# Kernel optimization log

Measured on AMD Instinct MI355X. Metric: run time of the kernel, lower is better.

Reference implementation:

```python
import jax, jax.numpy as jnp
import numpy as np

L = 12        # depth
DIM = 768     # model dim
HEADS = 12
DHEAD = 64
INNER = HEADS * DHEAD   # 768
MLP = 3072
P = 16        # patch size
IMG = 384
C = 3
B = 16
NCLS = 1000
NPATCH = (IMG // P) ** 2   # 576
N = NPATCH + 1             # 577 (cls token)
PATCH_DIM = C * P * P      # 768
SCALE = DIM ** (-0.5)      # NOTE: original scales by dim, not dim_head


def setup_inputs() -> dict:
    key = jax.random.key(0)
    ks = jax.random.split(key, 21)
    rn = lambda k, shape, s=0.02: jax.random.normal(k, shape, dtype=jnp.float32) * s
    return {
        "img": jax.random.normal(ks[0], (B, C, IMG, IMG), dtype=jnp.float32),
        "patch_w": rn(ks[1], (PATCH_DIM, DIM)),
        "patch_b": rn(ks[2], (DIM,)),
        "pos_emb": rn(ks[3], (1, N, DIM), 1.0),
        "cls_tok": rn(ks[4], (1, 1, DIM), 1.0),
        "ln1_w": jnp.ones((L, DIM), jnp.float32),
        "ln1_b": jnp.zeros((L, DIM), jnp.float32),
        "qkv_w": rn(ks[5], (L, DIM, 3 * INNER)),
        "out_w": rn(ks[6], (L, INNER, DIM)),
        "out_b": rn(ks[7], (L, DIM)),
        "ln2_w": jnp.ones((L, DIM), jnp.float32),
        "ln2_b": jnp.zeros((L, DIM), jnp.float32),
        "ff1_w": rn(ks[8], (L, DIM, MLP)),
        "ff1_b": rn(ks[9], (L, MLP)),
        "ff2_w": rn(ks[10], (L, MLP, DIM)),
        "ff2_b": rn(ks[11], (L, DIM)),
        "head_ln_w": jnp.ones((DIM,), jnp.float32),
        "head_ln_b": jnp.zeros((DIM,), jnp.float32),
        "head_w": rn(ks[12], (DIM, NCLS)),
        "head_b": rn(ks[13], (NCLS,)),
    }


def layer_norm(x, w, b, eps=1e-5):
    mu = jnp.mean(x, axis=-1, keepdims=True)
    var = jnp.mean(jnp.square(x - mu), axis=-1, keepdims=True)
    return (x - mu) * jax.lax.rsqrt(var + eps) * w + b


def _vit_forward(img, patch_w, patch_b, pos_emb, cls_tok,
                 ln1_w, ln1_b, qkv_w, out_w, out_b,
                 ln2_w, ln2_b, ff1_w, ff1_b, ff2_w, ff2_b,
                 head_ln_w, head_ln_b, head_w, head_b):
    b = img.shape[0]
    g = IMG // P
    # rearrange 'b c (h p1) (w p2) -> b (h w) (p1 p2 c)'
    x = img.reshape(b, C, g, P, g, P).transpose(0, 2, 4, 3, 5, 1).reshape(b, NPATCH, PATCH_DIM)
    x = x @ patch_w + patch_b                           # [b, 576, dim]
    cls = jnp.broadcast_to(cls_tok, (b, 1, DIM))
    x = jnp.concatenate([cls, x], axis=1) + pos_emb[:, :N]   # [b, 577, dim]

    def block(x, p):
        l1w, l1b, qkvw, ow, ob, l2w, l2b, f1w, f1b, f2w, f2b = p
        # attention (pre-norm, residual inside Attention.forward)
        h = layer_norm(x, l1w, l1b)
        qkv = h @ qkvw                                  # [b, n, 3*inner]
        q, k, v = jnp.split(qkv, 3, axis=-1)
        to_heads = lambda t: t.reshape(b, N, HEADS, DHEAD).transpose(0, 2, 1, 3)
        q, k, v = to_heads(q), to_heads(k), to_heads(v)  # [b, h, n, d]
        dots = jnp.einsum('bhid,bhjd->bhij', q, k) * SCALE
        attn = jax.nn.softmax(dots, axis=-1)
        o = jnp.einsum('bhij,bhjd->bhid', attn, v)
        o = o.transpose(0, 2, 1, 3).reshape(b, N, INNER)
        x = x + (o @ ow + ob)
        # feedforward (pre-norm, residual)
        h2 = layer_norm(x, l2w, l2b)
        h2 = jax.nn.gelu(h2 @ f1w + f1b, approximate=False)
        x = x + (h2 @ f2w + f2b)
        return x, None

    x, _ = jax.lax.scan(block, x,
                        (ln1_w, ln1_b, qkv_w, out_w, out_b,
                         ln2_w, ln2_b, ff1_w, ff1_b, ff2_w, ff2_b))
    cls_out = x[:, 0]                                   # [b, dim]
    return layer_norm(cls_out, head_ln_w, head_ln_b) @ head_w + head_b


def reference(img, patch_w, patch_b, pos_emb, cls_tok,
              ln1_w, ln1_b, qkv_w, out_w, out_b,
              ln2_w, ln2_b, ff1_w, ff1_b, ff2_w, ff2_b,
              head_ln_w, head_ln_b, head_w, head_b):
    return _vit_forward(img, patch_w, patch_b, pos_emb, cls_tok,
                        ln1_w, ln1_b, qkv_w, out_w, out_b,
                        ln2_w, ln2_b, ff1_w, ff1_b, ff2_w, ff2_b,
                        head_ln_w, head_ln_b, head_w, head_b)
```

## Files before the change

### kernel.cpp

```cpp
#include <hip/hip_runtime.h>
#include <cstdint>


typedef __attribute__((ext_vector_type(8))) short bf16x8;
typedef __attribute__((ext_vector_type(4))) float f32x4;

#define NTOK 577

__device__ __forceinline__ ushort f2bf(float f) {
  union { float f; unsigned int u; } x; x.f = f;
  unsigned int r = x.u + 0x7fffu + ((x.u >> 16) & 1u);
  return (ushort)(r >> 16);
}

__device__ __forceinline__ void gload_lds16(const ushort* g, ushort* l) {
  __builtin_amdgcn_global_load_lds(
      (const __attribute__((address_space(1))) unsigned int*)g,
      (__attribute__((address_space(3))) unsigned int*)l, 16, 0, 0);
}

__global__ __launch_bounds__(256) void convt_kernel(const float* __restrict__ W,
                                                    ushort* __restrict__ Wt,
                                                    int K, int N) {
  __shared__ float t[32][33];
  const int kb = blockIdx.x * 32, nb = blockIdx.y * 32;
  const int tx = threadIdx.x & 31, ty = threadIdx.x >> 5;
#pragma unroll
  for (int i = 0; i < 32; i += 8)
    t[ty + i][tx] = W[(size_t)(kb + ty + i) * N + (nb + tx)];
  __syncthreads();
#pragma unroll
  for (int i = 0; i < 32; i += 8)
    Wt[(size_t)(nb + ty + i) * K + (kb + tx)] = f2bf(t[tx][ty + i]);
}

__global__ __launch_bounds__(256) void im2col_kernel(const float* __restrict__ img,
                                                     ushort* __restrict__ Ap) {
  const int idx = blockIdx.x * 256 + threadIdx.x;
  const int j = idx % 768;
  const int m = idx / 768;
  const int c = j % 3;
  const int q = j / 3;
  const int px = q & 15, py = q >> 4;
  const int b = m / 576, p = m % 576;
  const int gy = p / 24, gx = p % 24;
  const float v = img[((size_t)(b * 3 + c) * 384 + (gy * 16 + py)) * 384 + (gx * 16 + px)];
  Ap[idx] = f2bf(v);
}

__global__ void clspos_kernel(const float* __restrict__ cls_tok,
                              const float* __restrict__ pos,
                              float* __restrict__ x) {
  const int i = blockIdx.x * 256 + threadIdx.x;
  const int b = i / 768, d = i % 768;
  x[(size_t)b * NTOK * 768 + d] = cls_tok[d] + pos[d];
}

__global__ __launch_bounds__(64) void ln_kernel(const float* __restrict__ x,
                                                const float* __restrict__ w,
                                                const float* __restrict__ bb,
                                                ushort* __restrict__ out) {
  const int row = blockIdx.x, lane = threadIdx.x;
  const float4* xr = reinterpret_cast<const float4*>(x + (size_t)row * 768);
  const float4 v0 = xr[lane], v1 = xr[lane + 64], v2 = xr[lane + 128];
  float vals[12] = {v0.x, v0.y, v0.z, v0.w, v1.x, v1.y, v1.z, v1.w,
                    v2.x, v2.y, v2.z, v2.w};
  float s = 0.f;
#pragma unroll
  for (int i = 0; i < 12; ++i) s += vals[i];
#pragma unroll
  for (int o = 32; o; o >>= 1) s += __shfl_xor(s, o);
  const float mu = s * (1.0f / 768.0f);
  float q = 0.f;
#pragma unroll
  for (int i = 0; i < 12; ++i) { const float d = vals[i] - mu; q += d * d; }
#pragma unroll
  for (int o = 32; o; o >>= 1) q += __shfl_xor(q, o);
  const float rstd = rsqrtf(q * (1.0f / 768.0f) + 1e-5f);
  const float4* w4 = reinterpret_cast<const float4*>(w);
  const float4* b4 = reinterpret_cast<const float4*>(bb);
  ushort* orow = out + (size_t)row * 768;
#pragma unroll
  for (int ch = 0; ch < 3; ++ch) {
    const float4 wv = w4[lane + ch * 64];
    const float4 bv = b4[lane + ch * 64];
    ushort4 u;
    u.x = f2bf((vals[ch * 4 + 0] - mu) * rstd * wv.x + bv.x);
    u.y = f2bf((vals[ch * 4 + 1] - mu) * rstd * wv.y + bv.y);
    u.z = f2bf((vals[ch * 4 + 2] - mu) * rstd * wv.z + bv.z);
    u.w = f2bf((vals[ch * 4 + 3] - mu) * rstd * wv.w + bv.w);
    *reinterpret_cast<ushort4*>(orow + ch * 256 + lane * 4) = u;
  }
}

constexpr int EPI_BF16 = 0;
constexpr int EPI_GELU_BF16 = 1;
constexpr int EPI_RES_F32 = 2;
constexpr int EPI_PATCH = 3;

template <int EPI>
__global__ __launch_bounds__(256) void gemm_kernel(
    const ushort* __restrict__ A, const ushort* __restrict__ Bt,
    const float* __restrict__ bias, const float* __restrict__ extra,
    void* __restrict__ Cptr, int M, int N, int K) {
  __shared__ ushort Alds[128 * 32];
  __shared__ ushort Blds[128 * 32];
  const int tid = threadIdx.x;
  const int tileM = blockIdx.x * 128, tileN = blockIdx.y * 128;
  const int wave = tid >> 6, lane = tid & 63;
  const int wrow = (wave >> 1) * 64, wcol = (wave & 1) * 64;
  const int lr = lane & 15, lk = (lane >> 4) * 8;

  f32x4 acc[4][4];
#pragma unroll
  for (int m = 0; m < 4; ++m)
#pragma unroll
    for (int n = 0; n < 4; ++n) acc[m][n] = (f32x4){0.f, 0.f, 0.f, 0.f};

  const int srow = wave * 32 + (lane >> 2);
  const int scol = (lane & 3) * 8;
  const ushort* Ap = A + (size_t)(tileM + srow) * K + scol;
  const ushort* Bp = Bt + (size_t)(tileN + srow) * K + scol;
  ushort* Al0 = &Alds[(wave * 2 + 0) * 512];
  ushort* Al1 = &Alds[(wave * 2 + 1) * 512];
  ushort* Bl0 = &Blds[(wave * 2 + 0) * 512];
  ushort* Bl1 = &Blds[(wave * 2 + 1) * 512];
  const size_t cstride = (size_t)16 * K;

  for (int k0 = 0; k0 < K; k0 += 32) {
    __syncthreads();
    gload_lds16(Ap + k0, Al0);
    gload_lds16(Ap + k0 + cstride, Al1);
    gload_lds16(Bp + k0, Bl0);
    gload_lds16(Bp + k0 + cstride, Bl1);
    __syncthreads();

    bf16x8 af[4], bfr[4];
#pragma unroll
    for (int m = 0; m < 4; ++m)
      af[m] = *reinterpret_cast<const bf16x8*>(&Alds[(wrow + m * 16 + lr) * 32 + lk]);
#pragma unroll
    for (int n = 0; n < 4; ++n)
      bfr[n] = *reinterpret_cast<const bf16x8*>(&Blds[(wcol + n * 16 + lr) * 32 + lk]);
#pragma unroll
    for (int m = 0; m < 4; ++m)
#pragma unroll
      for (int n = 0; n < 4; ++n)
        acc[m][n] = __builtin_amdgcn_mfma_f32_16x16x32_bf16(af[m], bfr[n],
                                                            acc[m][n], 0, 0, 0);
  }

  const int lr4 = (lane >> 4) * 4;
#pragma unroll
  for (int m = 0; m < 4; ++m) {
#pragma unroll
    for (int r = 0; r < 4; ++r) {
      const int row = tileM + wrow + m * 16 + lr4 + r;
      if (row >= M) continue;
#pragma unroll
      for (int n = 0; n < 4; ++n) {
        const int col = tileN + wcol + n * 16 + lr;
        float v = acc[m][n][r];
        if constexpr (EPI == EPI_BF16) {
          reinterpret_cast<ushort*>(Cptr)[(size_t)row * N + col] = f2bf(v);
        } else if constexpr (EPI == EPI_GELU_BF16) {
          v += bias[col];
          v = 0.5f * v * (1.0f + erff(v * 0.70710678118654752440f));
          reinterpret_cast<ushort*>(Cptr)[(size_t)row * N + col] = f2bf(v);
        } else if constexpr (EPI == EPI_RES_F32) {
          v += bias[col] + extra[(size_t)row * N + col];
          reinterpret_cast<float*>(Cptr)[(size_t)row * N + col] = v;
        } else {
          const int bb = row / 576;
          const int p = row - bb * 576;
          v += bias[col] + extra[(size_t)(p + 1) * 768 + col];
          reinterpret_cast<float*>(Cptr)[(size_t)(row + bb + 1) * 768 + col] = v;
        }
      }
    }
  }
}

__global__ __launch_bounds__(256) void attn_kernel(const ushort* __restrict__ qkv,
                                                   ushort* __restrict__ o) {
  __shared__ ushort sK[64][72];
  __shared__ ushort sVt[64][72];
  __shared__ ushort sP[4][16][72];
  const int bh = blockIdx.x;
  const int b = bh / 12, hh = bh % 12;
  const int q0 = blockIdx.y * 64;
  const int tid = threadIdx.x;
  const int wave = tid >> 6, lane = tid & 63;
  const int lr = lane & 15;
  const int lg = lane >> 4;
  const ushort* base = qkv + (size_t)b * NTOK * 2304 + hh * 64;
  const float SC = 0.03608439182435161f;

  bf16x8 qf[2];
  {
    const int qrow = q0 + wave * 16 + lr;
    if (qrow < NTOK) {
      const ushort* qp = base + (size_t)qrow * 2304 + lg * 8;
      qf[0] = *reinterpret_cast<const bf16x8*>(qp);
      qf[1] = *reinterpret_cast<const bf16x8*>(qp + 32);
    } else {
      qf[0] = (bf16x8){0, 0, 0, 0, 0, 0, 0, 0};
      qf[1] = qf[0];
    }
  }

  float mst[4], lst[4];
  f32x4 oacc[4];
#pragma unroll
  for (int i = 0; i < 4; ++i) {
    mst[i] = -1e30f; lst[i] = 0.f;
    oacc[i] = (f32x4){0.f, 0.f, 0.f, 0.f};
  }

  const int skey = tid >> 2;
  const int sd = (tid & 3) * 16;

  for (int t0 = 0; t0 < NTOK; t0 += 64) {
    __syncthreads();
    {
      const int gk = t0 + skey;
      int4 k0v, k1v, v0v, v1v;
      if (gk < NTOK) {
        const int4* kp = reinterpret_cast<const int4*>(base + (size_t)gk * 2304 + 768 + sd);
        k0v = kp[0]; k1v = kp[1];
        const int4* vp = reinterpret_cast<const int4*>(base + (size_t)gk * 2304 + 1536 + sd);
        v0v = vp[0]; v1v = vp[1];
      } else {
        int4 z; z.x = z.y = z.z = z.w = 0;
        k0v = k1v = v0v = v1v = z;
      }
      *reinterpret_cast<int4*>(&sK[skey][sd]) = k0v;
      *reinterpret_cast<int4*>(&sK[skey][sd + 8]) = k1v;
      const ushort* vs = reinterpret_cast<const ushort*>(&v0v);
#pragma unroll
      for (int i = 0; i < 8; ++i) sVt[sd + i][skey] = vs[i];
      const ushort* vs2 = reinterpret_cast<const ushort*>(&v1v);
#pragma unroll
      for (int i = 0; i < 8; ++i) sVt[sd + 8 + i][skey] = vs2[i];
    }
    __syncthreads();

    f32x4 sacc[4];
#pragma unroll
    for (int n = 0; n < 4; ++n) sacc[n] = (f32x4){0.f, 0.f, 0.f, 0.f};
#pragma unroll
    for (int n = 0; n < 4; ++n) {
      const bf16x8 kf0 = *reinterpret_cast<const bf16x8*>(&sK[n * 16 + lr][lg * 8]);
      const bf16x8 kf1 = *reinterpret_cast<const bf16x8*>(&sK[n * 16 + lr][32 + lg * 8]);
      sacc[n] = __builtin_amdgcn_mfma_f32_16x16x32_bf16(qf[0], kf0, sacc[n], 0, 0, 0);
      sacc[n] = __builtin_amdgcn_mfma_f32_16x16x32_bf16(qf[1], kf1, sacc[n], 0, 0, 0);
    }

    float s[4][4], pm[4];
#pragma unroll
    for (int reg = 0; reg < 4; ++reg) pm[reg] = -1e30f;
#pragma unroll
    for (int n = 0; n < 4; ++n)
#pragma unroll
      for (int reg = 0; reg < 4; ++reg) {
        float v = sacc[n][reg] * SC;
        if (t0 + n * 16 + lr >= NTOK) v = -1e30f;
        s[n][reg] = v;
        pm[reg] = fmaxf(pm[reg], v);
      }
#pragma unroll
    for (int off = 1; off < 16; off <<= 1)
#pragma unroll
      for (int reg = 0; reg < 4; ++reg) pm[reg] = fmaxf(pm[reg], __shfl_xor(pm[reg], off));

    float al[4], rs[4];
#pragma unroll
    for (int reg = 0; reg < 4; ++reg) {
      const float mn = fmaxf(mst[reg], pm[reg]);
      al[reg] = __expf(mst[reg] - mn);
      mst[reg] = mn;
      rs[reg] = 0.f;
    }
#pragma unroll
    for (int n = 0; n < 4; ++n)
#pragma unroll
      for (int reg = 0; reg < 4; ++reg) {
        s[n][reg] = __expf(s[n][reg] - mst[reg]);
        rs[reg] += s[n][reg];
      }
#pragma unroll
    for (int off = 1; off < 16; off <<= 1)
#pragma unroll
      for (int reg = 0; reg < 4; ++reg) rs[reg] += __shfl_xor(rs[reg], off);
#pragma unroll
    for (int reg = 0; reg < 4; ++reg) {
      lst[reg] = lst[reg] * al[reg] + rs[reg];
#pragma unroll
      for (int n = 0; n < 4; ++n) oacc[n][reg] *= al[reg];
    }

#pragma unroll
    for (int n = 0; n < 4; ++n)
#pragma unroll
      for (int reg = 0; reg < 4; ++reg)
        sP[wave][lg * 4 + reg][n * 16 + lr] = f2bf(s[n][reg]);

    const bf16x8 pf0 = *reinterpret_cast<const bf16x8*>(&sP[wave][lr][lg * 8]);
    const bf16x8 pf1 = *reinterpret_cast<const bf16x8*>(&sP[wave][lr][32 + lg * 8]);
#pragma unroll
    for (int n = 0; n < 4; ++n) {
      const bf16x8 vf0 = *reinterpret_cast<const bf16x8*>(&sVt[n * 16 + lr][lg * 8]);
      const bf16x8 vf1 = *reinterpret_cast<const bf16x8*>(&sVt[n * 16 + lr][32 + lg * 8]);
      oacc[n] = __builtin_amdgcn_mfma_f32_16x16x32_bf16(pf0, vf0, oacc[n], 0, 0, 0);
      oacc[n] = __builtin_amdgcn_mfma_f32_16x16x32_bf16(pf1, vf1, oacc[n], 0, 0, 0);
    }
  }

#pragma unroll
  for (int reg = 0; reg < 4; ++reg) {
    const int q = q0 + wave * 16 + lg * 4 + reg;
    if (q >= NTOK) continue;
    const float inv = 1.0f / lst[reg];
    ushort* op = o + (size_t)(b * NTOK + q) * 768 + hh * 64;
#pragma unroll
    for (int n = 0; n < 4; ++n) op[n * 16 + lr] = f2bf(oacc[n][reg] * inv);
  }
}

__global__ __launch_bounds__(256) void head_kernel(const float* __restrict__ x,
                                                   const float* __restrict__ lw,
                                                   const float* __restrict__ lb,
                                                   const float* __restrict__ hw,
                                                   const float* __restrict__ hb,
                                                   float* __restrict__ out) {
  __shared__ float srow[768];
  __shared__ float sred[8];
  const int b = blockIdx.x, tid = threadIdx.x;
  const float* xr = x + (size_t)b * NTOK * 768;
  for (int i = tid; i < 768; i += 256) srow[i] = xr[i];
  __syncthreads();
  float part = srow[tid] + srow[tid + 256] + srow[tid + 512];
#pragma unroll
  for (int off = 32; off; off >>= 1) part += __shfl_xor(part, off);
  if ((tid & 63) == 0) sred[tid >> 6] = part;
  __syncthreads();
  const float mu = (sred[0] + sred[1] + sred[2] + sred[3]) * (1.0f / 768.0f);
  const float d0 = srow[tid] - mu, d1 = srow[tid + 256] - mu, d2 = srow[tid + 512] - mu;
  float vp = d0 * d0 + d1 * d1 + d2 * d2;
#pragma unroll
  for (int off = 32; off; off >>= 1) vp += __shfl_xor(vp, off);
  if ((tid & 63) == 0) sred[4 + (tid >> 6)] = vp;
  __syncthreads();
  const float rstd = rsqrtf((sred[4] + sred[5] + sred[6] + sred[7]) * (1.0f / 768.0f) + 1e-5f);
  for (int i = tid; i < 768; i += 256) srow[i] = (srow[i] - mu) * rstd * lw[i] + lb[i];
  __syncthreads();
  const int c = blockIdx.y * 250 + tid;
  if (tid < 250 && c < 1000) {
    float a = 0.f;
#pragma unroll 4
    for (int k = 0; k < 768; ++k) a += srow[k] * hw[(size_t)k * 1000 + c];
    out[b * 1000 + c] = a + hb[c];
  }
}

extern "C" void kernel_launch(void* const* d_in, const int* in_sizes, int n_in,
                              void* d_out, int out_size, void* d_ws, size_t ws_size,
                              hipStream_t stream) {
  const float* img     = (const float*)d_in[0];
  const float* patch_w = (const float*)d_in[1];
  const float* patch_b = (const float*)d_in[2];
  const float* pos_emb = (const float*)d_in[3];
  const float* cls_tok = (const float*)d_in[4];
  const float* ln1_w   = (const float*)d_in[5];
  const float* ln1_b   = (const float*)d_in[6];
  const float* qkv_w   = (const float*)d_in[7];
  const float* out_w   = (const float*)d_in[8];
  const float* out_b   = (const float*)d_in[9];
  const float* ln2_w   = (const float*)d_in[10];
  const float* ln2_b   = (const float*)d_in[11];
  const float* ff1_w   = (const float*)d_in[12];
  const float* ff1_b   = (const float*)d_in[13];
  const float* ff2_w   = (const float*)d_in[14];
  const float* ff2_b   = (const float*)d_in[15];
  const float* hln_w   = (const float*)d_in[16];
  const float* hln_b   = (const float*)d_in[17];
  const float* head_w  = (const float*)d_in[18];
  const float* head_b  = (const float*)d_in[19];
  float* outp = (float*)d_out;

  char* wsp = (char*)d_ws;
  auto alloc = [&](size_t bytes) {
    char* p = wsp;
    wsp += (bytes + 255) & ~(size_t)255;
    return p;
  };
  float*  x    = (float*) alloc((size_t)9232 * 768 * 4);
  ushort* h    = (ushort*)alloc((size_t)9232 * 768 * 2);
  ushort* qkvb = (ushort*)alloc((size_t)9232 * 2304 * 2);
  ushort* mlp  = (ushort*)alloc((size_t)9232 * 3072 * 2);
  ushort* wq   = (ushort*)alloc((size_t)768 * 2304 * 2);
  ushort* wo   = (ushort*)alloc((size_t)768 * 768 * 2);
  ushort* w1   = (ushort*)alloc((size_t)768 * 3072 * 2);
  ushort* w2   = (ushort*)alloc((size_t)3072 * 768 * 2);
  ushort* apatch = mlp;
  ushort* wpatch = wq;

  convt_kernel<<<dim3(24, 24), 256, 0, stream>>>(patch_w, wpatch, 768, 768);
  im2col_kernel<<<27648, 256, 0, stream>>>(img, apatch);
  gemm_kernel<EPI_PATCH><<<dim3(72, 6), 256, 0, stream>>>(
      apatch, wpatch, patch_b, pos_emb, x, 9216, 768, 768);
  clspos_kernel<<<48, 256, 0, stream>>>(cls_tok, pos_emb, x);

  for (int l = 0; l < 12; ++l) {
    ln_kernel<<<9232, 64, 0, stream>>>(x, ln1_w + l * 768, ln1_b + l * 768, h);
    convt_kernel<<<dim3(24, 72), 256, 0, stream>>>(qkv_w + (size_t)l * 768 * 2304, wq, 768, 2304);
    gemm_kernel<EPI_BF16><<<dim3(73, 18), 256, 0, stream>>>(
        h, wq, nullptr, nullptr, qkvb, 9232, 2304, 768);
    attn_kernel<<<dim3(192, 10), 256, 0, stream>>>(qkvb, h);
    convt_kernel<<<dim3(24, 24), 256, 0, stream>>>(out_w + (size_t)l * 768 * 768, wo, 768, 768);
    gemm_kernel<EPI_RES_F32><<<dim3(73, 6), 256, 0, stream>>>(
        h, wo, out_b + l * 768, x, x, 9232, 768, 768);
    ln_kernel<<<9232, 64, 0, stream>>>(x, ln2_w + l * 768, ln2_b + l * 768, h);
    convt_kernel<<<dim3(24, 96), 256, 0, stream>>>(ff1_w + (size_t)l * 768 * 3072, w1, 768, 3072);
    gemm_kernel<EPI_GELU_BF16><<<dim3(73, 24), 256, 0, stream>>>(
        h, w1, ff1_b + l * 3072, nullptr, mlp, 9232, 3072, 768);
    convt_kernel<<<dim3(96, 24), 256, 0, stream>>>(ff2_w + (size_t)l * 3072 * 768, w2, 3072, 768);
    gemm_kernel<EPI_RES_F32><<<dim3(73, 6), 256, 0, stream>>>(
        mlp, w2, ff2_b + l * 768, x, x, 9232, 768, 3072);
  }

  head_kernel<<<dim3(16, 4), 256, 0, stream>>>(x, hln_w, hln_b, head_w, head_b, outp);
}
```

Baseline: 4.966 ms.

## Add 256x256 eight-wave pipelined GEMM for QKV/FF1 and swizzle attention LDS

Adds a new 512-thread GEMM kernel with 256x256 tiles, double-buffered direct global-to-LDS loads, an XOR-style swizzled LDS layout, explicit waitcnt/barrier scheduling interleaved with MFMA phases, and XCD-aware workgroup remapping. It is used for the QKV and FF1 projections. The attention kernel's K and V-transposed shared buffers switch from padded rows to a swizzled layout to cut bank conflicts. The goal is higher MFMA utilisation and data reuse in the largest GEMMs. In exchange the M tail is computed past row 9232, since the 37 M-tiles cover 9472 rows and only the stores are bounds-checked. That relies on the oversized buffers and adds register pressure.

```diff
diff --git a/kernel.cpp b/kernel.cpp
--- a/kernel.cpp
+++ b/kernel.cpp
@@ -17,6 +17,17 @@
   __builtin_amdgcn_global_load_lds(
       (const __attribute__((address_space(1))) unsigned int*)g,
       (__attribute__((address_space(3))) unsigned int*)l, 16, 0, 0);
+}
+
+#define VMCNT4 asm volatile("s_waitcnt vmcnt(4)" ::: "memory")
+#define VMCNT2 asm volatile("s_waitcnt vmcnt(2)" ::: "memory")
+#define VMCNT0 asm volatile("s_waitcnt vmcnt(0)" ::: "memory")
+#define LGKM0  asm volatile("s_waitcnt lgkmcnt(0)" ::: "memory")
+#define SCHED0 __builtin_amdgcn_sched_barrier(0)
+#define BARRIER __builtin_amdgcn_s_barrier()
+
+__device__ __forceinline__ int gsw(int row) {
+  return (row & 7) + 2 * ((row >> 4) & 3);
 }
 
 __global__ __launch_bounds__(256) void convt_kernel(const float* __restrict__ W,
@@ -97,6 +108,184 @@
 constexpr int EPI_GELU_BF16 = 1;
 constexpr int EPI_RES_F32 = 2;
 constexpr int EPI_PATCH = 3;
+
+template <int EPI>
+__global__ __launch_bounds__(512, 2) void gemm8_kernel(
+    const ushort* __restrict__ A, const ushort* __restrict__ Bt,
+    const float* __restrict__ bias, void* __restrict__ Cptr,
+    int M, int N, int K, int mt) {
+  __shared__ ushort lds[2][2][16384];
+
+  const int nwg = gridDim.x;
+  const int orig = blockIdx.x;
+  const int q8 = nwg >> 3, r8 = nwg & 7, xcd = orig & 7, sidx = orig >> 3;
+  const int wg = (xcd < r8 ? xcd * (q8 + 1) : r8 * (q8 + 1) + (xcd - r8) * q8) + sidx;
+  const int tileM = (wg % mt) * 256;
+  const int tileN = (wg / mt) * 256;
+
+  const int tid = threadIdx.x;
+  const int wave = tid >> 6, lane = tid & 63;
+  const int wm = wave >> 2, wn = wave & 3;
+  const int lr = lane & 15, lg = lane >> 4;
+
+  f32x4 acc[8][4];
+#pragma unroll
+  for (int i = 0; i < 8; ++i)
+#pragma unroll
+    for (int j = 0; j < 4; ++j) acc[i][j] = (f32x4){0.f, 0.f, 0.f, 0.f};
+
+  int rsA[2][2], rsB[2][2];
+  const ushort* pA[2][2];
+  const ushort* pB[2][2];
+#pragma unroll
+  for (int h = 0; h < 2; ++h)
+#pragma unroll
+    for (int g = 0; g < 2; ++g) {
+      const int c = wave * 2 + g;
+      {
+        const int rowst = h * 64 + ((c >> 3) << 7) + ((c & 7) << 3);
+        rsA[h][g] = rowst;
+        const int row = rowst + (lane >> 3);
+        const int lgr = ((lane & 7) - gsw(row)) & 7;
+        pA[h][g] = A + (size_t)(tileM + row) * K + lgr * 8;
+      }
+      {
+        const int rowst = h * 32 + ((c >> 2) << 6) + ((c & 3) << 3);
+        rsB[h][g] = rowst;
+        const int row = rowst + (lane >> 3);
+        const int lgr = ((lane & 7) - gsw(row)) & 7;
+        pB[h][g] = Bt + (size_t)(tileN + row) * K + lgr * 8;
+      }
+    }
+
+#define STAGE_A(h, buf, k1)                                   \
+  gload_lds16(pA[h][0] + (k1), &lds[buf][0][rsA[h][0] * 64]); \
+  gload_lds16(pA[h][1] + (k1), &lds[buf][0][rsA[h][1] * 64]);
+#define STAGE_B(h, buf, k1)                                   \
+  gload_lds16(pB[h][0] + (k1), &lds[buf][1][rsB[h][0] * 64]); \
+  gload_lds16(pB[h][1] + (k1), &lds[buf][1][rsB[h][1] * 64]);
+
+  bf16x8 areg[8], breg[4];
+#define LDA8(h, buf)                                                          \
+  {                                                                           \
+    const ushort* base = &lds[buf][0][0];                                     \
+    _Pragma("unroll") for (int mf = 0; mf < 4; ++mf) {                        \
+      const int row = wm * 128 + (h) * 64 + mf * 16 + lr;                     \
+      _Pragma("unroll") for (int ks = 0; ks < 2; ++ks) {                      \
+        const int pg = (ks * 4 + lg + (lr & 7) + 2 * mf) & 7;                 \
+        areg[mf * 2 + ks] =                                                   \
+            *reinterpret_cast<const bf16x8*>(&base[row * 64 + pg * 8]);       \
+      }                                                                       \
+    }                                                                         \
+  }
+#define LDB4(q, buf)                                                          \
+  {                                                                           \
+    const ushort* base = &lds[buf][1][0];                                     \
+    _Pragma("unroll") for (int nf = 0; nf < 2; ++nf) {                        \
+      const int row = wn * 64 + (q) * 32 + nf * 16 + lr;                      \
+      _Pragma("unroll") for (int ks = 0; ks < 2; ++ks) {                      \
+        const int pg = (ks * 4 + lg + (lr & 7) + 2 * (((q)*2 + nf) & 3)) & 7; \
+        breg[nf * 2 + ks] =                                                   \
+            *reinterpret_cast<const bf16x8*>(&base[row * 64 + pg * 8]);       \
+      }                                                                       \
+    }                                                                         \
+  }
+#define MFMA16(h, q)                                                        \
+  __builtin_amdgcn_s_setprio(1);                                            \
+  _Pragma("unroll") for (int mf = 0; mf < 4; ++mf)                          \
+      _Pragma("unroll") for (int nf = 0; nf < 2; ++nf)                      \
+          _Pragma("unroll") for (int ks = 0; ks < 2; ++ks)                  \
+              acc[(h)*4 + mf][(q)*2 + nf] =                                 \
+                  __builtin_amdgcn_mfma_f32_16x16x32_bf16(                  \
+                      areg[mf * 2 + ks], breg[nf * 2 + ks],                 \
+                      acc[(h)*4 + mf][(q)*2 + nf], 0, 0, 0);                \
+  __builtin_amdgcn_s_setprio(0);
+
+  STAGE_A(0, 0, 0);
+  STAGE_B(0, 0, 0);
+  STAGE_A(1, 0, 0);
+  STAGE_B(1, 0, 0);
+
+  const int NT = K >> 6;
+  for (int t = 0; t < NT - 1; ++t) {
+    const int cb = t & 1, nb = (t + 1) & 1;
+    const int k1 = (t + 1) * 64;
+    VMCNT4; SCHED0;
+    BARRIER;
+    LDA8(0, cb);
+    LDB4(0, cb);
+    STAGE_A(0, nb, k1);
+    LGKM0; SCHED0;
+    MFMA16(0, 0);
+    VMCNT4; SCHED0;
+    BARRIER;
+    LDA8(1, cb);
+    STAGE_B(0, nb, k1);
+    LGKM0; SCHED0;
+    MFMA16(1, 0);
+    VMCNT4; SCHED0;
+    BARRIER;
+    LDB4(1, cb);
+    STAGE_A(1, nb, k1);
+    LGKM0; SCHED0;
+    MFMA16(1, 1);
+    BARRIER;
+    LDA8(0, cb);
+    STAGE_B(1, nb, k1);
+    LGKM0; SCHED0;
+    MFMA16(0, 1);
+  }
+
+  {
+    const int cb = (NT - 1) & 1;
+    VMCNT4; SCHED0;
+    BARRIER;
+    LDA8(0, cb);
+    LDB4(0, cb);
+    LGKM0; SCHED0;
+    MFMA16(0, 0);
+    VMCNT2; SCHED0;
+    BARRIER;
+    LDA8(1, cb);
+    LGKM0; SCHED0;
+    MFMA16(1, 0);
+    VMCNT0; SCHED0;
+    BARRIER;
+    LDB4(1, cb);
+    LGKM0; SCHED0;
+    MFMA16(1, 1);
+    BARRIER;
+    LDA8(0, cb);
+    LGKM0; SCHED0;
+    MFMA16(0, 1);
+  }
+
+#pragma unroll
+  for (int am = 0; am < 8; ++am) {
+#pragma unroll
+    for (int r = 0; r < 4; ++r) {
+      const int row = tileM + wm * 128 + (am >> 2) * 64 + (am & 3) * 16 + lg * 4 + r;
+      if (row >= M) continue;
+#pragma unroll
+      for (int an = 0; an < 4; ++an) {
+        const int col = tileN + wn * 64 + (an >> 1) * 32 + (an & 1) * 16 + lr;
+        float v = acc[am][an][r];
+        if constexpr (EPI == EPI_BF16) {
+          reinterpret_cast<ushort*>(Cptr)[(size_t)row * N + col] = f2bf(v);
+        } else {
+          v += bias[col];
+          v = 0.5f * v * (1.0f + erff(v * 0.70710678118654752440f));
+          reinterpret_cast<ushort*>(Cptr)[(size_t)row * N + col] = f2bf(v);
+        }
+      }
+    }
+  }
+#undef STAGE_A
+#undef STAGE_B
+#undef LDA8
+#undef LDB4
+#undef MFMA16
+}
 
 template <int EPI>
 __global__ __launch_bounds__(256) void gemm_kernel(
@@ -183,9 +372,9 @@
 
 __global__ __launch_bounds__(256) void attn_kernel(const ushort* __restrict__ qkv,
                                                    ushort* __restrict__ o) {
-  __shared__ ushort sK[64][72];
-  __shared__ ushort sVt[64][72];
-  __shared__ ushort sP[4][16][72];
+  __shared__ ushort sK[64 * 64];
+  __shared__ ushort sVt[64 * 64];
+  __shared__ ushort sP[4][16 * 72];
   const int bh = blockIdx.x;
   const int b = bh / 12, hh = bh % 12;
   const int q0 = blockIdx.y * 64;
@@ -218,7 +407,8 @@
   }
 
   const int skey = tid >> 2;
-  const int sd = (tid & 3) * 16;
+  const int sc4 = tid & 3;
+  const int gswk = gsw(skey);
 
   for (int t0 = 0; t0 < NTOK; t0 += 64) {
     __syncthreads();
@@ -226,22 +416,27 @@
       const int gk = t0 + skey;
       int4 k0v, k1v, v0v, v1v;
       if (gk < NTOK) {
-        const int4* kp = reinterpret_cast<const int4*>(base + (size_t)gk * 2304 + 768 + sd);
+        const int4* kp = reinterpret_cast<const int4*>(base + (size_t)gk * 2304 + 768 + sc4 * 16);
         k0v = kp[0]; k1v = kp[1];
-        const int4* vp = reinterpret_cast<const int4*>(base + (size_t)gk * 2304 + 1536 + sd);
+        const int4* vp = reinterpret_cast<const int4*>(base + (size_t)gk * 2304 + 1536 + sc4 * 16);
         v0v = vp[0]; v1v = vp[1];
       } else {
         int4 z; z.x = z.y = z.z = z.w = 0;
         k0v = k1v = v0v = v1v = z;
       }
-      *reinterpret_cast<int4*>(&sK[skey][sd]) = k0v;
-      *reinterpret_cast<int4*>(&sK[skey][sd + 8]) = k1v;
+      *reinterpret_cast<int4*>(&sK[skey * 64 + (((2 * sc4 + 0) + gswk) & 7) * 8]) = k0v;
+      *reinterpret_cast<int4*>(&sK[skey * 64 + (((2 * sc4 + 1) + gswk) & 7) * 8]) = k1v;
       const ushort* vs = reinterpret_cast<const ushort*>(&v0v);
-#pragma unroll
-      for (int i = 0; i < 8; ++i) sVt[sd + i][skey] = vs[i];
       const ushort* vs2 = reinterpret_cast<const ushort*>(&v1v);
 #pragma unroll
-      for (int i = 0; i < 8; ++i) sVt[sd + 8 + i][skey] = vs2[i];
+      for (int i = 0; i < 8; ++i) {
+        const int d0 = sc4 * 16 + i;
+        const int pg0 = ((skey >> 3) + gsw(d0)) & 7;
+        sVt[d0 * 64 + pg0 * 8 + (skey & 7)] = vs[i];
+        const int d1 = sc4 * 16 + 8 + i;
+        const int pg1 = ((skey >> 3) + gsw(d1)) & 7;
+        sVt[d1 * 64 + pg1 * 8 + (skey & 7)] = vs2[i];
+      }
     }
     __syncthreads();
 
@@ -250,8 +445,10 @@
     for (int n = 0; n < 4; ++n) sacc[n] = (f32x4){0.f, 0.f, 0.f, 0.f};
 #pragma unroll
     for (int n = 0; n < 4; ++n) {
-      const bf16x8 kf0 = *reinterpret_cast<const bf16x8*>(&sK[n * 16 + lr][lg * 8]);
-      const bf16x8 kf1 = *reinterpret_cast<const bf16x8*>(&sK[n * 16 + lr][32 + lg * 8]);
+      const int row = n * 16 + lr;
+      const int rot = (lr & 7) + 2 * n;
+      const bf16x8 kf0 = *reinterpret_cast<const bf16x8*>(&sK[row * 64 + ((lg + rot) & 7) * 8]);
+      const bf16x8 kf1 = *reinterpret_cast<const bf16x8*>(&sK[row * 64 + ((4 + lg + rot) & 7) * 8]);
       sacc[n] = __builtin_amdgcn_mfma_f32_16x16x32_bf16(qf[0], kf0, sacc[n], 0, 0, 0);
       sacc[n] = __builtin_amdgcn_mfma_f32_16x16x32_bf16(qf[1], kf1, sacc[n], 0, 0, 0);
     }
@@ -303,14 +500,16 @@
     for (int n = 0; n < 4; ++n)
 #pragma unroll
       for (int reg = 0; reg < 4; ++reg)
-        sP[wave][lg * 4 + reg][n * 16 + lr] = f2bf(s[n][reg]);
-
-    const bf16x8 pf0 = *reinterpret_cast<const bf16x8*>(&sP[wave][lr][lg * 8]);
-    const bf16x8 pf1 = *reinterpret_cast<const bf16x8*>(&sP[wave][lr][32 + lg * 8]);
+        sP[wave][(lg * 4 + reg) * 72 + n * 16 + lr] = f2bf(s[n][reg]);
+
+    const bf16x8 pf0 = *reinterpret_cast<const bf16x8*>(&sP[wave][lr * 72 + lg * 8]);
+    const bf16x8 pf1 = *reinterpret_cast<const bf16x8*>(&sP[wave][lr * 72 + 32 + lg * 8]);
 #pragma unroll
     for (int n = 0; n < 4; ++n) {
-      const bf16x8 vf0 = *reinterpret_cast<const bf16x8*>(&sVt[n * 16 + lr][lg * 8]);
-      const bf16x8 vf1 = *reinterpret_cast<const bf16x8*>(&sVt[n * 16 + lr][32 + lg * 8]);
+      const int row = n * 16 + lr;
+      const int rot = (lr & 7) + 2 * n;
+      const bf16x8 vf0 = *reinterpret_cast<const bf16x8*>(&sVt[row * 64 + ((lg + rot) & 7) * 8]);
+      const bf16x8 vf1 = *reinterpret_cast<const bf16x8*>(&sVt[row * 64 + ((4 + lg + rot) & 7) * 8]);
       oacc[n] = __builtin_amdgcn_mfma_f32_16x16x32_bf16(pf0, vf0, oacc[n], 0, 0, 0);
       oacc[n] = __builtin_amdgcn_mfma_f32_16x16x32_bf16(pf1, vf1, oacc[n], 0, 0, 0);
     }
@@ -414,16 +613,16 @@
   for (int l = 0; l < 12; ++l) {
     ln_kernel<<<9232, 64, 0, stream>>>(x, ln1_w + l * 768, ln1_b + l * 768, h);
     convt_kernel<<<dim3(24, 72), 256, 0, stream>>>(qkv_w + (size_t)l * 768 * 2304, wq, 768, 2304);
-    gemm_kernel<EPI_BF16><<<dim3(73, 18), 256, 0, stream>>>(
-        h, wq, nullptr, nullptr, qkvb, 9232, 2304, 768);
+    gemm8_kernel<EPI_BF16><<<37 * 9, 512, 0, stream>>>(
+        h, wq, nullptr, qkvb, 9232, 2304, 768, 37);
     attn_kernel<<<dim3(192, 10), 256, 0, stream>>>(qkvb, h);
     convt_kernel<<<dim3(24, 24), 256, 0, stream>>>(out_w + (size_t)l * 768 * 768, wo, 768, 768);
     gemm_kernel<EPI_RES_F32><<<dim3(73, 6), 256, 0, stream>>>(
         h, wo, out_b + l * 768, x, x, 9232, 768, 768);
     ln_kernel<<<9232, 64, 0, stream>>>(x, ln2_w + l * 768, ln2_b + l * 768, h);
     convt_kernel<<<dim3(24, 96), 256, 0, stream>>>(ff1_w + (size_t)l * 768 * 3072, w1, 768, 3072);
-    gemm_kernel<EPI_GELU_BF16><<<dim3(73, 24), 256, 0, stream>>>(
-        h, w1, ff1_b + l * 3072, nullptr, mlp, 9232, 3072, 768);
+    gemm8_kernel<EPI_GELU_BF16><<<37 * 12, 512, 0, stream>>>(
+        h, w1, ff1_b + l * 3072, mlp, 9232, 3072, 768, 37);
     convt_kernel<<<dim3(96, 24), 256, 0, stream>>>(ff2_w + (size_t)l * 3072 * 768, w2, 3072, 768);
     gemm_kernel<EPI_RES_F32><<<dim3(73, 6), 256, 0, stream>>>(
         mlp, w2, ff2_b + l * 768, x, x, 9232, 768, 3072);
```

Result: faster. 4.638 ms (-6.6%).
